# Kernel tuning notes

Hardware: AMD Instinct MI355X
Metric: run time of the kernel (lower is better)

Reference implementation:

```python
import jax, jax.numpy as jnp
import numpy as np

ALPHA = 0.2
NEG_INF = -9e15


def setup_inputs() -> dict:
    key = jax.random.key(0)
    k1, k2, k3, k4 = jax.random.split(key, 4)
    N, F_IN, F_OUT, H = 4096, 1, 64, 12
    x = jax.random.normal(k1, (N, F_IN), dtype=jnp.float32)
    adj = jax.random.randint(k2, (N, N), 0, 2).astype(jnp.int32)
    # per-head params stacked: W [H, F_IN, F_OUT], a [H, 2*F_OUT, 1]
    W = jax.random.normal(k3, (H, F_IN, F_OUT), dtype=jnp.float32) * 0.1
    a = jax.random.normal(k4, (H, 2 * F_OUT, 1), dtype=jnp.float32) * 0.1
    return {"x": x, "adj": adj, "W": W, "a": a}


def reference(x, adj, W, a):
    # h per head: [H, N, F_OUT]
    h = jnp.einsum('nf,hfo->hno', x, W)
    F_out = h.shape[-1]
    # a_input[i,j] = concat(h_i, h_j), so a_input @ a = h_i.a_src + h_j.a_dst
    a_src = a[:, :F_out, 0]   # [H, F_OUT]
    a_dst = a[:, F_out:, 0]   # [H, F_OUT]
    e_src = jnp.einsum('hnf,hf->hn', h, a_src)  # [H, N]
    e_dst = jnp.einsum('hnf,hf->hn', h, a_dst)  # [H, N]
    e = jax.nn.leaky_relu(e_src[:, :, None] + e_dst[:, None, :], ALPHA)  # [H,N,N]
    e = jnp.where(adj[None] > 0, e, NEG_INF)
    attn = jax.nn.softmax(e, axis=-1)           # softmax over neighbors j
    h_prime = jnp.einsum('hij,hjf->hif', attn, h)  # [H, N, F_OUT]
    # concat heads along feature dim -> [N, H*F_OUT]
    N = h_prime.shape[1]
    return jnp.transpose(h_prime, (1, 0, 2)).reshape(N, -1)
```

## Files before the change

### kernel.cpp

```cpp
#include <hip/hip_runtime.h>

#define GAT_H 12
#define GAT_N 4096
#define GAT_F 64
#define LOG2E 1.4426950408889634f


__device__ float g_tab2[GAT_H * GAT_N];
__device__ float g_sd[2 * GAT_H + 1];

__global__ __launch_bounds__(256) void gat_prep(const float* __restrict__ W,
                                                const float* __restrict__ a,
                                                const float* __restrict__ x) {
    const int b    = blockIdx.x;
    const int tid  = threadIdx.x;
    const int lane = tid & 63;
    const int wave = tid >> 6;

    if (b < GAT_H) {
        if (wave == 0) {
            const float wf = W[b * GAT_F + lane];
            float ps = wf * a[b * 2 * GAT_F + lane];
            float pd = wf * a[b * 2 * GAT_F + GAT_F + lane];
            #pragma unroll
            for (int off = 32; off > 0; off >>= 1) {
                ps += __shfl_xor(ps, off, 64);
                pd += __shfl_xor(pd, off, 64);
            }
            if (lane == 0) { g_sd[b] = ps; g_sd[GAT_H + b] = pd; }
        }
        return;
    }
    if (b == GAT_H) {
        if (wave == 0) {
            float s = 0.0f;
            #pragma unroll
            for (int j = 0; j < GAT_N / 64; ++j) s += x[j * 64 + lane];
            #pragma unroll
            for (int off = 32; off > 0; off >>= 1) s += __shfl_xor(s, off, 64);
            if (lane == 0) g_sd[2 * GAT_H] = s * (1.0f / GAT_N);
        }
        return;
    }

    const int bt    = b - (GAT_H + 1);
    const int h     = bt >> 2;
    const int chunk = bt & 3;
    const float wf  = W[h * GAT_F + lane];
    float pd = wf * a[h * 2 * GAT_F + GAT_F + lane];
    #pragma unroll
    for (int off = 32; off > 0; off >>= 1) pd += __shfl_xor(pd, off, 64);
    const float dl5 = 0.2f * pd * LOG2E;
    #pragma unroll
    for (int k = 0; k < 4; ++k) {
        const int j = chunk * 1024 + k * 256 + tid;
        g_tab2[h * GAT_N + j] = __builtin_amdgcn_exp2f(dl5 * x[j]);
    }
}

__global__ __launch_bounds__(512) void gat_main(const float* __restrict__ x,
                                                const int* __restrict__ adj,
                                                const float* __restrict__ W,
                                                float* __restrict__ out) {
    __shared__ float tab_lds[2][GAT_H][256];
    __shared__ float cbuf[8][GAT_H];

    const int tid   = threadIdx.x;
    const int row0  = blockIdx.x * 8;
    const int lane  = tid & 63;
    const int wave  = tid >> 6;
    const int rp    = wave >> 1;
    const int hg    = wave & 1;
    const int hbase = hg * 6;
    const int rowA  = row0 + rp * 2;

    float rho[2][6];
    #pragma unroll
    for (int r = 0; r < 2; ++r) {
        const float xr = x[rowA + r];
        #pragma unroll
        for (int hh = 0; hh < 6; ++hh)
            rho[r][hh] = __uint_as_float(__builtin_amdgcn_readfirstlane(
                __float_as_uint(__builtin_amdgcn_exp2f(
                    -0.8f * LOG2E * xr * g_sd[hbase + hh]))));
    }

    float den[2][6], num[2][6];
    #pragma unroll
    for (int r = 0; r < 2; ++r)
        #pragma unroll
        for (int hh = 0; hh < 6; ++hh) { den[r][hh] = 0.0f; num[r][hh] = 0.0f; }

    const float2* __restrict__ tg = (const float2*)g_tab2;
    int sh[3], sj[3];
    #pragma unroll
    for (int k = 0; k < 3; ++k) {
        const int p = k * 512 + tid;
        sh[k] = p >> 7;
        sj[k] = p & 127;
    }
    float2* __restrict__ lds2 = (float2*)tab_lds;

    #pragma unroll
    for (int k = 0; k < 3; ++k)
        lds2[sh[k] * 128 + sj[k]] = tg[sh[k] * (GAT_N / 2) + sj[k]];
    const int4*   __restrict__ a4p0 = (const int4*)(adj + (size_t)rowA * GAT_N);
    const int4*   __restrict__ a4p1 = a4p0 + (GAT_N / 4);
    const float4* __restrict__ x4   = (const float4*)x;

    int4   aP0[2], aP1[2];
    float4 xP[2];
    aP0[0] = a4p0[lane];      aP1[0] = a4p1[lane];      xP[0] = x4[lane];
    aP0[1] = a4p0[64 + lane]; aP1[1] = a4p1[64 + lane]; xP[1] = x4[64 + lane];
    __syncthreads();

    #pragma unroll 2
    for (int it = 0; it < 16; ++it) {
        const int buf = it & 1;

        float am[2][4], axj[2][4];
        {
            const int*   ai0 = (const int*)&aP0[buf];
            const int*   ai1 = (const int*)&aP1[buf];
            const float* xp  = (const float*)&xP[buf];
            #pragma unroll
            for (int e = 0; e < 4; ++e) {
                am[0][e]  = (float)ai0[e];
                am[1][e]  = (float)ai1[e];
                axj[0][e] = am[0][e] * xp[e];
                axj[1][e] = am[1][e] * xp[e];
            }
        }

        const int n1 = (it < 15) ? it + 1 : 15;
        float2 st[3];
        #pragma unroll
        for (int k = 0; k < 3; ++k)
            st[k] = tg[sh[k] * (GAT_N / 2) + n1 * 128 + sj[k]];

        const int n2i = ((it < 14) ? it + 2 : 15) * 64 + lane;
        aP0[buf] = a4p0[n2i];
        aP1[buf] = a4p1[n2i];
        xP[buf]  = x4[n2i];

        #pragma unroll
        for (int hh = 0; hh < 6; ++hh) {
            const float4 e2v = *(const float4*)&tab_lds[buf][hbase + hh][4 * lane];
            const float* e2  = (const float*)&e2v;
            #pragma unroll
            for (int e = 0; e < 4; ++e) {
                const float w  = e2[e] * e2[e];
                const float w4 = w * w;
                const float p0 = fmaxf(w4, rho[0][hh]) * e2[e];
                const float p1 = fmaxf(w4, rho[1][hh]) * e2[e];
                den[0][hh] = fmaf(p0, am[0][e],  den[0][hh]);
                num[0][hh] = fmaf(p0, axj[0][e], num[0][hh]);
                den[1][hh] = fmaf(p1, am[1][e],  den[1][hh]);
                num[1][hh] = fmaf(p1, axj[1][e], num[1][hh]);
            }
        }

        #pragma unroll
        for (int k = 0; k < 3; ++k)
            lds2[(buf ^ 1) * (GAT_H * 128) + sh[k] * 128 + sj[k]] = st[k];
        __syncthreads();
    }

    #pragma unroll
    for (int r = 0; r < 2; ++r) {
        #pragma unroll
        for (int hh = 0; hh < 6; ++hh) {
            float d = den[r][hh], n = num[r][hh];
            #pragma unroll
            for (int off = 32; off > 0; off >>= 1) {
                d += __shfl_xor(d, off, 64);
                n += __shfl_xor(n, off, 64);
            }
            if (lane == 0)
                cbuf[rp * 2 + r][hbase + hh] =
                    d > 0.0f ? n / d : g_sd[2 * GAT_H];
        }
    }
    __syncthreads();

    #pragma unroll
    for (int rr = 0; rr < 8; ++rr) {
        const size_t base = (size_t)(row0 + rr) * (GAT_H * GAT_F);
        #pragma unroll
        for (int k = 0; k < 2; ++k) {
            const int pos = k * 512 + tid;
            if (pos < GAT_H * GAT_F)
                out[base + pos] = cbuf[rr][pos >> 6] * W[pos];
        }
    }
}

extern "C" void kernel_launch(void* const* d_in, const int* in_sizes, int n_in,
                              void* d_out, int out_size, void* d_ws, size_t ws_size,
                              hipStream_t stream) {
    const float* x   = (const float*)d_in[0];
    const int*   adj = (const int*)d_in[1];
    const float* W   = (const float*)d_in[2];
    const float* a   = (const float*)d_in[3];
    float* out = (float*)d_out;
    (void)d_ws; (void)ws_size;

    gat_prep<<<GAT_H + 1 + 48, 256, 0, stream>>>(W, a, x);
    gat_main<<<GAT_N / 8, 512, 0, stream>>>(x, adj, W, out);
}
```

Baseline: 128.8 us.

## Preload full per-head exp table into LDS and split blocks over head groups

Each block now covers 32 rows and 3 heads instead of 8 rows and all 12 heads. It loads the whole 3-head exp table (48KB) into LDS once, which removes the per-iteration global table streaming and the per-iteration __syncthreads. Each wave handles 4 rows, so each table value loaded from LDS is reused across more rows. The cost is that every adjacency row is now read by 4 different blocks (4x adj traffic, possibly served from L2), along with larger LDS use per block, which may reduce occupancy.

```diff
diff --git a/kernel.cpp b/kernel.cpp
--- a/kernel.cpp
+++ b/kernel.cpp
@@ -3,6 +3,8 @@
 #define GAT_H 12
 #define GAT_N 4096
 #define GAT_F 64
+#define BR 32
+#define BH 3
 #define LOG2E 1.4426950408889634f
 
 
@@ -62,114 +64,102 @@
                                                 const int* __restrict__ adj,
                                                 const float* __restrict__ W,
                                                 float* __restrict__ out) {
-    __shared__ float tab_lds[2][GAT_H][256];
-    __shared__ float cbuf[8][GAT_H];
+    __shared__ float tabs[BH][GAT_N];
+    __shared__ float cbuf[BR][BH];
 
-    const int tid   = threadIdx.x;
-    const int row0  = blockIdx.x * 8;
-    const int lane  = tid & 63;
-    const int wave  = tid >> 6;
-    const int rp    = wave >> 1;
-    const int hg    = wave & 1;
-    const int hbase = hg * 6;
-    const int rowA  = row0 + rp * 2;
+    const int tid  = threadIdx.x;
+    const int lane = tid & 63;
+    const int wid  = tid >> 6;
+    const int hb   = (blockIdx.x & 3) * BH;
+    const int row0 = (blockIdx.x >> 2) * BR;
+    const int rA   = row0 + wid * 4;
 
-    float rho[2][6];
+    const float4* __restrict__ tg4 = (const float4*)(g_tab2 + hb * GAT_N);
+    float4* ls4 = (float4*)tabs;
     #pragma unroll
-    for (int r = 0; r < 2; ++r) {
-        const float xr = x[rowA + r];
+    for (int k = 0; k < (BH * GAT_N / 4) / 512; ++k)
+        ls4[k * 512 + tid] = tg4[k * 512 + tid];
+
+    float rho[4][BH];
+    #pragma unroll
+    for (int r = 0; r < 4; ++r) {
+        const float xr = x[rA + r];
         #pragma unroll
-        for (int hh = 0; hh < 6; ++hh)
+        for (int hh = 0; hh < BH; ++hh)
             rho[r][hh] = __uint_as_float(__builtin_amdgcn_readfirstlane(
                 __float_as_uint(__builtin_amdgcn_exp2f(
-                    -0.8f * LOG2E * xr * g_sd[hbase + hh]))));
+                    -0.8f * LOG2E * xr * g_sd[hb + hh]))));
     }
 
-    float den[2][6], num[2][6];
+    float den[4][BH], num[4][BH];
     #pragma unroll
-    for (int r = 0; r < 2; ++r)
+    for (int r = 0; r < 4; ++r)
         #pragma unroll
-        for (int hh = 0; hh < 6; ++hh) { den[r][hh] = 0.0f; num[r][hh] = 0.0f; }
+        for (int hh = 0; hh < BH; ++hh) { den[r][hh] = 0.0f; num[r][hh] = 0.0f; }
 
-    const float2* __restrict__ tg = (const float2*)g_tab2;
-    int sh[3], sj[3];
+    const int4*   __restrict__ a4 = (const int4*)(adj + (size_t)rA * GAT_N);
+    const float4* __restrict__ x4 = (const float4*)x;
+
+    int4   aP[2][4];
+    float4 xP[2];
     #pragma unroll
-    for (int k = 0; k < 3; ++k) {
-        const int p = k * 512 + tid;
-        sh[k] = p >> 7;
-        sj[k] = p & 127;
+    for (int r = 0; r < 4; ++r) {
+        aP[0][r] = a4[r * (GAT_N / 4) + lane];
+        aP[1][r] = a4[r * (GAT_N / 4) + 64 + lane];
     }
-    float2* __restrict__ lds2 = (float2*)tab_lds;
+    xP[0] = x4[lane];
+    xP[1] = x4[64 + lane];
 
-    #pragma unroll
-    for (int k = 0; k < 3; ++k)
-        lds2[sh[k] * 128 + sj[k]] = tg[sh[k] * (GAT_N / 2) + sj[k]];
-    const int4*   __restrict__ a4p0 = (const int4*)(adj + (size_t)rowA * GAT_N);
-    const int4*   __restrict__ a4p1 = a4p0 + (GAT_N / 4);
-    const float4* __restrict__ x4   = (const float4*)x;
-
-    int4   aP0[2], aP1[2];
-    float4 xP[2];
-    aP0[0] = a4p0[lane];      aP1[0] = a4p1[lane];      xP[0] = x4[lane];
-    aP0[1] = a4p0[64 + lane]; aP1[1] = a4p1[64 + lane]; xP[1] = x4[64 + lane];
     __syncthreads();
 
     #pragma unroll 2
     for (int it = 0; it < 16; ++it) {
         const int buf = it & 1;
 
-        float am[2][4], axj[2][4];
-        {
-            const int*   ai0 = (const int*)&aP0[buf];
-            const int*   ai1 = (const int*)&aP1[buf];
-            const float* xp  = (const float*)&xP[buf];
+        int4   aC[4];
+        float4 xC = xP[buf];
+        #pragma unroll
+        for (int r = 0; r < 4; ++r) aC[r] = aP[buf][r];
+
+        const int n2i = ((it < 14) ? it + 2 : 15) * 64 + lane;
+        #pragma unroll
+        for (int r = 0; r < 4; ++r) aP[buf][r] = a4[r * (GAT_N / 4) + n2i];
+        xP[buf] = x4[n2i];
+
+        float4 e2v[BH];
+        #pragma unroll
+        for (int hh = 0; hh < BH; ++hh)
+            e2v[hh] = *(const float4*)&tabs[hh][it * 256 + 4 * lane];
+
+        const float* xp = (const float*)&xC;
+        #pragma unroll
+        for (int e = 0; e < 4; ++e) {
+            float am[4], axj[4];
             #pragma unroll
-            for (int e = 0; e < 4; ++e) {
-                am[0][e]  = (float)ai0[e];
-                am[1][e]  = (float)ai1[e];
-                axj[0][e] = am[0][e] * xp[e];
-                axj[1][e] = am[1][e] * xp[e];
+            for (int r = 0; r < 4; ++r) {
+                const int ai = ((const int*)&aC[r])[e];
+                am[r]  = (float)ai;
+                axj[r] = am[r] * xp[e];
+            }
+            #pragma unroll
+            for (int hh = 0; hh < BH; ++hh) {
+                const float ev = ((const float*)&e2v[hh])[e];
+                const float w  = ev * ev;
+                const float w4 = w * w;
+                #pragma unroll
+                for (int r = 0; r < 4; ++r) {
+                    const float p = fmaxf(w4, rho[r][hh]) * ev;
+                    den[r][hh] = fmaf(p, am[r],  den[r][hh]);
+                    num[r][hh] = fmaf(p, axj[r], num[r][hh]);
+                }
             }
         }
-
-        const int n1 = (it < 15) ? it + 1 : 15;
-        float2 st[3];
-        #pragma unroll
-        for (int k = 0; k < 3; ++k)
-            st[k] = tg[sh[k] * (GAT_N / 2) + n1 * 128 + sj[k]];
-
-        const int n2i = ((it < 14) ? it + 2 : 15) * 64 + lane;
-        aP0[buf] = a4p0[n2i];
-        aP1[buf] = a4p1[n2i];
-        xP[buf]  = x4[n2i];
-
-        #pragma unroll
-        for (int hh = 0; hh < 6; ++hh) {
-            const float4 e2v = *(const float4*)&tab_lds[buf][hbase + hh][4 * lane];
-            const float* e2  = (const float*)&e2v;
-            #pragma unroll
-            for (int e = 0; e < 4; ++e) {
-                const float w  = e2[e] * e2[e];
-                const float w4 = w * w;
-                const float p0 = fmaxf(w4, rho[0][hh]) * e2[e];
-                const float p1 = fmaxf(w4, rho[1][hh]) * e2[e];
-                den[0][hh] = fmaf(p0, am[0][e],  den[0][hh]);
-                num[0][hh] = fmaf(p0, axj[0][e], num[0][hh]);
-                den[1][hh] = fmaf(p1, am[1][e],  den[1][hh]);
-                num[1][hh] = fmaf(p1, axj[1][e], num[1][hh]);
-            }
-        }
-
-        #pragma unroll
-        for (int k = 0; k < 3; ++k)
-            lds2[(buf ^ 1) * (GAT_H * 128) + sh[k] * 128 + sj[k]] = st[k];
-        __syncthreads();
     }
 
     #pragma unroll
-    for (int r = 0; r < 2; ++r) {
+    for (int r = 0; r < 4; ++r) {
         #pragma unroll
-        for (int hh = 0; hh < 6; ++hh) {
+        for (int hh = 0; hh < BH; ++hh) {
             float d = den[r][hh], n = num[r][hh];
             #pragma unroll
             for (int off = 32; off > 0; off >>= 1) {
@@ -177,21 +167,18 @@
                 n += __shfl_xor(n, off, 64);
             }
             if (lane == 0)
-                cbuf[rp * 2 + r][hbase + hh] =
-                    d > 0.0f ? n / d : g_sd[2 * GAT_H];
+                cbuf[wid * 4 + r][hh] = d > 0.0f ? n / d : g_sd[2 * GAT_H];
         }
     }
     __syncthreads();
 
     #pragma unroll
-    for (int rr = 0; rr < 8; ++rr) {
-        const size_t base = (size_t)(row0 + rr) * (GAT_H * GAT_F);
-        #pragma unroll
-        for (int k = 0; k < 2; ++k) {
-            const int pos = k * 512 + tid;
-            if (pos < GAT_H * GAT_F)
-                out[base + pos] = cbuf[rr][pos >> 6] * W[pos];
-        }
+    for (int q = 0; q < BR * BH / 8; ++q) {
+        const int qq  = q * 8 + wid;
+        const int row = qq / BH;
+        const int hh  = qq - row * BH;
+        out[(size_t)(row0 + row) * (GAT_H * GAT_F) + (hb + hh) * GAT_F + lane] =
+            cbuf[row][hh] * W[(hb + hh) * GAT_F + lane];
     }
 }
 
@@ -206,5 +193,5 @@
     (void)d_ws; (void)ws_size;
 
     gat_prep<<<GAT_H + 1 + 48, 256, 0, stream>>>(W, a, x);
-    gat_main<<<GAT_N / 8, 512, 0, stream>>>(x, adj, W, out);
+    gat_main<<<(GAT_N / BR) * 4, 512, 0, stream>>>(x, adj, W, out);
 }
```

Measured after the change: 144.5 us. 12.2% more time.
